# Kernel tuning notes

Measured on AMD Instinct MI355X. Metric: run time of the kernel, lower is better.

## Reference

```python
import jax, jax.numpy as jnp
import numpy as np

EPS = 1e-5
DOWNSAMPLE = 0.5


def setup_inputs() -> dict:
    key = jax.random.key(0)
    k1, k2, k3 = jax.random.split(key, 3)
    B, C, H, W = 32, 256, 128, 128
    x = jax.random.normal(k1, (B, C, H, W), dtype=jnp.float32)
    # 1x1 conv: weight [3, C], bias [3]
    conv_w = jax.random.normal(k2, (3, C), dtype=jnp.float32) / np.sqrt(C).astype(np.float32)
    conv_b = jax.random.normal(k3, (3,), dtype=jnp.float32) * 0.01
    return {"x": x, "conv_w": conv_w, "conv_b": conv_b}


def reference(x, conv_w, conv_b):
    B, C, H, W = x.shape
    dh = int(round(H * DOWNSAMPLE))
    dw = int(round(W * DOWNSAMPLE))

    # 1x1 conv producing 3 channels: 2 offset + 1 attention logit
    oa = jnp.einsum('bchw,oc->bohw', x, conv_w) + conv_b[None, :, None, None]
    offset = oa[:, :2]                      # [B,2,H,W]
    attention = jnp.exp(oa[:, 2:3])         # [B,1,H,W]

    # normalized destination coordinates = base grid + offset, clamped
    gy = jnp.broadcast_to((jnp.arange(H, dtype=x.dtype) / H)[:, None], (H, W))
    gx = jnp.broadcast_to((jnp.arange(W, dtype=x.dtype) / W)[None, :], (H, W))
    base = jnp.stack([gy, gx])              # [2,H,W]
    dest = jnp.clip(base[None] + offset, 0.0, 1.0 - EPS)
    dy = jnp.floor(dest[:, 0] * dh)
    dx = jnp.floor(dest[:, 1] * dw)
    cell = (dy * dw + dx).astype(jnp.int32)  # [B,H,W] spatial cell index

    # full flat destination index over (batch, channel, cell)
    b_off = jnp.arange(B, dtype=jnp.int32)[:, None, None, None] * (C * dh * dw)
    c_off = jnp.arange(C, dtype=jnp.int32)[None, :, None, None] * (dh * dw)
    destination = cell[:, None] + b_off + c_off  # [B,C,H,W]

    # scatter-add attention-weighted features
    xw = (x * attention).reshape(-1)
    feat = jax.ops.segment_sum(xw, destination.reshape(-1), num_segments=B * C * dh * dw)

    # scatter-add attention per (batch, cell) for normalization
    a_idx = cell + jnp.arange(B, dtype=jnp.int32)[:, None, None] * (dh * dw)
    att_sum = jax.ops.segment_sum(attention.reshape(-1), a_idx.reshape(-1), num_segments=B * dh * dw) + EPS

    out = feat.reshape(B, C, dh, dw) / att_sum.reshape(B, 1, dh, dw)
    return (out, offset, destination)
```

## Files before the change

kernel.cpp:

```cpp
#include <hip/hip_runtime.h>
#include <math.h>

#define NB 32
#define NC 256
#define NH 128
#define NW 128
#define NDH 64
#define NDW 64
#define NHW (NH * NW)
#define NCELLS (NDH * NDW)
#define OUT0_N (NB * NC * NCELLS)
#define OUT1_BASE OUT0_N
#define OUT1_N (NB * 2 * NHW)
#define OUT2_BASE (OUT1_BASE + OUT1_N)

#define EPSF 1e-5f

typedef unsigned short u16;
typedef unsigned int   u32;

#define WS_CELLS   ((size_t)0)
#define WS_ATTS    (WS_CELLS + (size_t)NB*NHW*2)
#define WS_ECOMB   (WS_ATTS + (size_t)NB*NHW*4)
#define WS_ASUM    (WS_ECOMB + (size_t)NB*NHW*4)

__global__ __launch_bounds__(256) void k_conv(
    const float* __restrict__ x, const float* __restrict__ cw,
    const float* __restrict__ cb, float* __restrict__ out,
    u16* __restrict__ cells, float* __restrict__ atts)
{
    __shared__ float cwS[3][NC];
    __shared__ float red[256][13];
    __shared__ int   cellv[64];

    const int t    = threadIdx.x;
    const int blk  = blockIdx.x;
    const int b    = blk >> 8;
    const int tile = blk & 255;
    const int h    = tile >> 1;
    const int w0   = (tile & 1) << 6;
    const int pixbase = h * NW + w0;

    cwS[0][t] = cw[t];
    cwS[1][t] = cw[NC + t];
    cwS[2][t] = cw[2 * NC + t];
    __syncthreads();

    const int ct = t >> 4;
    const int pg = (t & 15) << 2;
    const float* xb = x + (size_t)b * NC * NHW + pixbase + pg;

    float p00 = 0, p01 = 0, p02 = 0;
    float p10 = 0, p11 = 0, p12 = 0;
    float p20 = 0, p21 = 0, p22 = 0;
    float p30 = 0, p31 = 0, p32 = 0;

    #pragma unroll
    for (int i = 0; i < 16; ++i) {
        const int c = (i << 4) + ct;
        const float4 xv = *reinterpret_cast<const float4*>(xb + (size_t)c * NHW);
        const float wc0 = cwS[0][c], wc1 = cwS[1][c], wc2 = cwS[2][c];
        p00 += xv.x * wc0; p01 += xv.x * wc1; p02 += xv.x * wc2;
        p10 += xv.y * wc0; p11 += xv.y * wc1; p12 += xv.y * wc2;
        p20 += xv.z * wc0; p21 += xv.z * wc1; p22 += xv.z * wc2;
        p30 += xv.w * wc0; p31 += xv.w * wc1; p32 += xv.w * wc2;
    }

    red[t][0]  = p00; red[t][1]  = p01; red[t][2]  = p02;
    red[t][3]  = p10; red[t][4]  = p11; red[t][5]  = p12;
    red[t][6]  = p20; red[t][7]  = p21; red[t][8]  = p22;
    red[t][9]  = p30; red[t][10] = p31; red[t][11] = p32;
    __syncthreads();

    if (t < 64) {
        const int px   = t;
        const int row0 = px >> 2;
        const int col  = (px & 3) * 3;
        float s0 = 0, s1 = 0, s2 = 0;
        #pragma unroll
        for (int j = 0; j < 16; ++j) {
            const int r = row0 + (j << 4);
            s0 += red[r][col];
            s1 += red[r][col + 1];
            s2 += red[r][col + 2];
        }
        const float off0 = s0 + cb[0];
        const float off1 = s1 + cb[1];
        const float att  = expf(s2 + cb[2]);

        const float gy = (float)h * (1.0f / NH);
        const float gx = (float)(w0 + px) * (1.0f / NW);
        const float dyf = fminf(fmaxf(gy + off0, 0.0f), 0.99999f);
        const float dxf = fminf(fmaxf(gx + off1, 0.0f), 0.99999f);
        const int dy = (int)floorf(dyf * (float)NDH);
        const int dx = (int)floorf(dxf * (float)NDW);
        const int cell = dy * NDW + dx;

        cellv[px] = cell;
        cells[b * NHW + pixbase + px] = (u16)cell;
        atts [b * NHW + pixbase + px] = att;

        const int o1 = OUT1_BASE + b * 2 * NHW + pixbase + px;
        out[o1]       = off0;
        out[o1 + NHW] = off1;
    }
    __syncthreads();

    const int  c0 = cellv[pg], c1 = cellv[pg + 1], c2 = cellv[pg + 2], c3 = cellv[pg + 3];
    float* __restrict__ dst = out + OUT2_BASE;
    #pragma unroll
    for (int i = 0; i < 16; ++i) {
        const int c = (i << 4) + ct;
        const int basec = (b * NC + c) * NCELLS;
        float4 dv;
        dv.x = (float)(basec + c0);
        dv.y = (float)(basec + c1);
        dv.z = (float)(basec + c2);
        dv.w = (float)(basec + c3);
        *reinterpret_cast<float4*>(dst + (size_t)(b * NC + c) * NHW + pixbase + pg) = dv;
    }
}

__global__ __launch_bounds__(1024) void k_sort(
    const u16* __restrict__ cells, const float* __restrict__ atts,
    u32* __restrict__ ecomb, float* __restrict__ asum)
{
    __shared__ u32   hist[NCELLS];
    __shared__ float as_[NCELLS];
    __shared__ u32   ts[1024];

    const int t = threadIdx.x;
    const int b = blockIdx.x;
    const u16*   cb_ = cells + b * NHW;
    const float* ab_ = atts + b * NHW;

    #pragma unroll
    for (int j = 0; j < 4; ++j) { hist[t + 1024 * j] = 0u; as_[t + 1024 * j] = 0.f; }
    __syncthreads();

    #pragma unroll
    for (int j = 0; j < 16; ++j) {
        const int p  = t + 1024 * j;
        const int cl = cb_[p];
        atomicAdd(&hist[cl], 1u);
        atomicAdd(&as_[cl], ab_[p]);
    }
    __syncthreads();

    const u32 h0 = hist[4 * t], h1 = hist[4 * t + 1], h2 = hist[4 * t + 2], h3 = hist[4 * t + 3];
    const u32 T  = h0 + h1 + h2 + h3;
    ts[t] = T;
    __syncthreads();
    for (int off = 1; off < 1024; off <<= 1) {
        const u32 v = (t >= off) ? ts[t - off] : 0u;
        __syncthreads();
        ts[t] += v;
        __syncthreads();
    }
    const u32 base = ts[t] - T;
    hist[4 * t]     = base;
    hist[4 * t + 1] = base + h0;
    hist[4 * t + 2] = base + h0 + h1;
    hist[4 * t + 3] = base + h0 + h1 + h2;

    #pragma unroll
    for (int j = 0; j < 4; ++j)
        asum[b * NCELLS + t + 1024 * j] = as_[t + 1024 * j];
    __syncthreads();

    #pragma unroll
    for (int j = 0; j < 16; ++j) {
        const int p  = t + 1024 * j;
        const int cl = cb_[p];
        const u32 pos = atomicAdd(&hist[cl], 1u);
        ecomb[b * NHW + pos] = ((u32)cl << 16) | (u32)p;
    }
}

__global__ __launch_bounds__(256) void k_gather(
    const float* __restrict__ x, const float* __restrict__ atts,
    const u32* __restrict__ ecomb, const float* __restrict__ asum,
    float* __restrict__ out)
{
    __shared__ float xpl[NHW];
    __shared__ float acc[NCELLS];

    const int t   = threadIdx.x;
    const int blk = blockIdx.x;
    const int b   = blk >> 8;
    const int c   = blk & 255;

    const float4* xp4  = reinterpret_cast<const float4*>(x + (size_t)(b * NC + c) * NHW);
    const float4* at4  = reinterpret_cast<const float4*>(atts + b * NHW);
    float4*       xpl4 = reinterpret_cast<float4*>(xpl);
    float4*       acc4 = reinterpret_cast<float4*>(acc);

    #pragma unroll
    for (int k = 0; k < 16; ++k) {
        float4 xv = xp4[t + 256 * k];
        const float4 av = at4[t + 256 * k];
        xv.x *= av.x; xv.y *= av.y; xv.z *= av.z; xv.w *= av.w;
        xpl4[t + 256 * k] = xv;
    }
    const float4 z4 = make_float4(0.f, 0.f, 0.f, 0.f);
    #pragma unroll
    for (int k = 0; k < 4; ++k) acc4[t + 256 * k] = z4;
    __syncthreads();

    const u32* el = ecomb + b * NHW + t * 64;
    float s   = 0.f;
    int   cur = (int)(el[0] >> 16);

    #define ACCUM(E, V)                                            \
        {                                                          \
            const int cl_ = (int)((E) >> 16);                      \
            if (cl_ != cur) { atomicAdd(&acc[cur], s); s = 0.f; cur = cl_; } \
            s += (V);                                              \
        }

    for (int ch = 0; ch < 8; ++ch) {
        const uint4 e0 = *reinterpret_cast<const uint4*>(el + ch * 8);
        const uint4 e1 = *reinterpret_cast<const uint4*>(el + ch * 8 + 4);
        const float v0 = xpl[e0.x & 0xFFFFu];
        const float v1 = xpl[e0.y & 0xFFFFu];
        const float v2 = xpl[e0.z & 0xFFFFu];
        const float v3 = xpl[e0.w & 0xFFFFu];
        const float v4 = xpl[e1.x & 0xFFFFu];
        const float v5 = xpl[e1.y & 0xFFFFu];
        const float v6 = xpl[e1.z & 0xFFFFu];
        const float v7 = xpl[e1.w & 0xFFFFu];
        ACCUM(e0.x, v0); ACCUM(e0.y, v1); ACCUM(e0.z, v2); ACCUM(e0.w, v3);
        ACCUM(e1.x, v4); ACCUM(e1.y, v5); ACCUM(e1.z, v6); ACCUM(e1.w, v7);
    }
    atomicAdd(&acc[cur], s);
    #undef ACCUM
    __syncthreads();

    const float4* as4 = reinterpret_cast<const float4*>(asum + b * NCELLS);
    float4* ob4 = reinterpret_cast<float4*>(out + (size_t)(b * NC + c) * NCELLS);
    #pragma unroll
    for (int k = 0; k < 4; ++k) {
        float4 a = acc4[t + 256 * k];
        const float4 sv = as4[t + 256 * k];
        a.x /= (sv.x + EPSF);
        a.y /= (sv.y + EPSF);
        a.z /= (sv.z + EPSF);
        a.w /= (sv.w + EPSF);
        ob4[t + 256 * k] = a;
    }
}

extern "C" void kernel_launch(void* const* d_in, const int* in_sizes, int n_in,
                              void* d_out, int out_size, void* d_ws, size_t ws_size,
                              hipStream_t stream)
{
    (void)in_sizes; (void)n_in; (void)out_size; (void)ws_size;
    const float* x  = (const float*)d_in[0];
    const float* cw = (const float*)d_in[1];
    const float* cb = (const float*)d_in[2];
    float* out = (float*)d_out;
    char*  ws  = (char*)d_ws;

    u16*   cells = (u16*)  (ws + WS_CELLS);
    float* atts  = (float*)(ws + WS_ATTS);
    u32*   ecomb = (u32*)  (ws + WS_ECOMB);
    float* asum  = (float*)(ws + WS_ASUM);

    k_conv  <<<dim3(NB * 256), dim3(256),  0, stream>>>(x, cw, cb, out, cells, atts);
    k_sort  <<<dim3(NB),       dim3(1024), 0, stream>>>(cells, atts, ecomb, asum);
    k_gather<<<dim3(NB * NC),  dim3(256),  0, stream>>>(x, atts, ecomb, asum, out);
}
```

Before: 463.7 us.

## Stage x directly to LDS asynchronously and fold attention into sorted entries

The gather kernel now copies the x plane into LDS with global_load_lds instead of loading, multiplying by attention and storing through registers. The attention weight is packed next to each sorted entry (8-byte entries), so the multiply happens at gather time. The sort kernel precomputes the reciprocal of the attention sum, so the final normalisation is a multiply instead of a divide. Each thread also runs four independent accumulation streams for more ILP, at the cost of doubling entry-list bandwidth and adding more LDS atomics at stream boundaries.

```diff
diff --git a/kernel.cpp b/kernel.cpp
--- a/kernel.cpp
+++ b/kernel.cpp
@@ -21,8 +21,15 @@
 
 #define WS_CELLS   ((size_t)0)
 #define WS_ATTS    (WS_CELLS + (size_t)NB*NHW*2)
-#define WS_ECOMB   (WS_ATTS + (size_t)NB*NHW*4)
-#define WS_ASUM    (WS_ECOMB + (size_t)NB*NHW*4)
+#define WS_ENTS    (WS_ATTS + (size_t)NB*NHW*4)
+#define WS_IASUM   (WS_ENTS + (size_t)NB*NHW*8)
+
+__device__ __forceinline__ void async_stage16(const float* g, float* l) {
+    __builtin_amdgcn_global_load_lds(
+        (const __attribute__((address_space(1))) unsigned int*)g,
+        (__attribute__((address_space(3))) unsigned int*)l,
+        16, 0, 0);
+}
 
 __global__ __launch_bounds__(256) void k_conv(
     const float* __restrict__ x, const float* __restrict__ cw,
@@ -123,7 +130,7 @@
 
 __global__ __launch_bounds__(1024) void k_sort(
     const u16* __restrict__ cells, const float* __restrict__ atts,
-    u32* __restrict__ ecomb, float* __restrict__ asum)
+    uint2* __restrict__ ents, float* __restrict__ iasum)
 {
     __shared__ u32   hist[NCELLS];
     __shared__ float as_[NCELLS];
@@ -164,8 +171,10 @@
     hist[4 * t + 3] = base + h0 + h1 + h2;
 
     #pragma unroll
-    for (int j = 0; j < 4; ++j)
-        asum[b * NCELLS + t + 1024 * j] = as_[t + 1024 * j];
+    for (int j = 0; j < 4; ++j) {
+        const int i = t + 1024 * j;
+        iasum[b * NCELLS + i] = 1.0f / (as_[i] + EPSF);
+    }
     __syncthreads();
 
     #pragma unroll
@@ -173,79 +182,83 @@
         const int p  = t + 1024 * j;
         const int cl = cb_[p];
         const u32 pos = atomicAdd(&hist[cl], 1u);
-        ecomb[b * NHW + pos] = ((u32)cl << 16) | (u32)p;
-    }
-}
-
-__global__ __launch_bounds__(256) void k_gather(
-    const float* __restrict__ x, const float* __restrict__ atts,
-    const u32* __restrict__ ecomb, const float* __restrict__ asum,
-    float* __restrict__ out)
+        ents[b * NHW + pos] = make_uint2(((u32)cl << 16) | (u32)p,
+                                         __float_as_uint(ab_[p]));
+    }
+}
+
+#define ENT(EX, EY, CUR, S)                                                   \
+    {                                                                         \
+        const int   cl_ = (int)((EX) >> 16);                                  \
+        const float v_  = xpl[(EX) & 0xFFFFu] * __uint_as_float(EY);          \
+        if (cl_ != (CUR)) { atomicAdd(&acc[(CUR)], (S)); (S) = 0.f; (CUR) = cl_; } \
+        (S) += v_;                                                            \
+    }
+
+__global__ __launch_bounds__(256) void k_gd(
+    const float* __restrict__ x, const uint2* __restrict__ ents,
+    const float* __restrict__ iasum, float* __restrict__ out)
 {
     __shared__ float xpl[NHW];
     __shared__ float acc[NCELLS];
 
-    const int t   = threadIdx.x;
-    const int blk = blockIdx.x;
-    const int b   = blk >> 8;
-    const int c   = blk & 255;
-
-    const float4* xp4  = reinterpret_cast<const float4*>(x + (size_t)(b * NC + c) * NHW);
-    const float4* at4  = reinterpret_cast<const float4*>(atts + b * NHW);
-    float4*       xpl4 = reinterpret_cast<float4*>(xpl);
-    float4*       acc4 = reinterpret_cast<float4*>(acc);
-
+    const int t    = threadIdx.x;
+    const int blk  = blockIdx.x;
+    const int b    = blk >> 8;
+    const int c    = blk & 255;
+    const int wave = t >> 6;
+    const int lane = t & 63;
+
+    const float* xp = x + (size_t)(b * NC + c) * NHW;
     #pragma unroll
     for (int k = 0; k < 16; ++k) {
-        float4 xv = xp4[t + 256 * k];
-        const float4 av = at4[t + 256 * k];
-        xv.x *= av.x; xv.y *= av.y; xv.z *= av.z; xv.w *= av.w;
-        xpl4[t + 256 * k] = xv;
-    }
+        const int vec = (k * 4 + wave) * 64 + lane;
+        async_stage16(xp + vec * 4, &xpl[vec * 4]);
+    }
+
+    float4* acc4 = reinterpret_cast<float4*>(acc);
     const float4 z4 = make_float4(0.f, 0.f, 0.f, 0.f);
     #pragma unroll
     for (int k = 0; k < 4; ++k) acc4[t + 256 * k] = z4;
-    __syncthreads();
-
-    const u32* el = ecomb + b * NHW + t * 64;
-    float s   = 0.f;
-    int   cur = (int)(el[0] >> 16);
-
-    #define ACCUM(E, V)                                            \
-        {                                                          \
-            const int cl_ = (int)((E) >> 16);                      \
-            if (cl_ != cur) { atomicAdd(&acc[cur], s); s = 0.f; cur = cl_; } \
-            s += (V);                                              \
+
+    __syncthreads();
+
+    {
+        const uint2* el = ents + b * NHW + t * 64;
+        float s0 = 0.f, s1 = 0.f, s2 = 0.f, s3 = 0.f;
+        int   c0 = (int)(el[0].x  >> 16);
+        int   c1 = (int)(el[16].x >> 16);
+        int   c2 = (int)(el[32].x >> 16);
+        int   c3 = (int)(el[48].x >> 16);
+
+        #pragma unroll
+        for (int i = 0; i < 8; ++i) {
+            const uint4 q0 = *reinterpret_cast<const uint4*>(el + 0  + i * 2);
+            const uint4 q1 = *reinterpret_cast<const uint4*>(el + 16 + i * 2);
+            const uint4 q2 = *reinterpret_cast<const uint4*>(el + 32 + i * 2);
+            const uint4 q3 = *reinterpret_cast<const uint4*>(el + 48 + i * 2);
+            ENT(q0.x, q0.y, c0, s0); ENT(q0.z, q0.w, c0, s0);
+            ENT(q1.x, q1.y, c1, s1); ENT(q1.z, q1.w, c1, s1);
+            ENT(q2.x, q2.y, c2, s2); ENT(q2.z, q2.w, c2, s2);
+            ENT(q3.x, q3.y, c3, s3); ENT(q3.z, q3.w, c3, s3);
         }
-
-    for (int ch = 0; ch < 8; ++ch) {
-        const uint4 e0 = *reinterpret_cast<const uint4*>(el + ch * 8);
-        const uint4 e1 = *reinterpret_cast<const uint4*>(el + ch * 8 + 4);
-        const float v0 = xpl[e0.x & 0xFFFFu];
-        const float v1 = xpl[e0.y & 0xFFFFu];
-        const float v2 = xpl[e0.z & 0xFFFFu];
-        const float v3 = xpl[e0.w & 0xFFFFu];
-        const float v4 = xpl[e1.x & 0xFFFFu];
-        const float v5 = xpl[e1.y & 0xFFFFu];
-        const float v6 = xpl[e1.z & 0xFFFFu];
-        const float v7 = xpl[e1.w & 0xFFFFu];
-        ACCUM(e0.x, v0); ACCUM(e0.y, v1); ACCUM(e0.z, v2); ACCUM(e0.w, v3);
-        ACCUM(e1.x, v4); ACCUM(e1.y, v5); ACCUM(e1.z, v6); ACCUM(e1.w, v7);
-    }
-    atomicAdd(&acc[cur], s);
-    #undef ACCUM
-    __syncthreads();
-
-    const float4* as4 = reinterpret_cast<const float4*>(asum + b * NCELLS);
+        atomicAdd(&acc[c0], s0);
+        atomicAdd(&acc[c1], s1);
+        atomicAdd(&acc[c2], s2);
+        atomicAdd(&acc[c3], s3);
+    }
+    __syncthreads();
+
+    const float4* ia4 = reinterpret_cast<const float4*>(iasum + b * NCELLS);
     float4* ob4 = reinterpret_cast<float4*>(out + (size_t)(b * NC + c) * NCELLS);
     #pragma unroll
     for (int k = 0; k < 4; ++k) {
         float4 a = acc4[t + 256 * k];
-        const float4 sv = as4[t + 256 * k];
-        a.x /= (sv.x + EPSF);
-        a.y /= (sv.y + EPSF);
-        a.z /= (sv.z + EPSF);
-        a.w /= (sv.w + EPSF);
+        const float4 sv = ia4[t + 256 * k];
+        a.x *= sv.x;
+        a.y *= sv.y;
+        a.z *= sv.z;
+        a.w *= sv.w;
         ob4[t + 256 * k] = a;
     }
 }
@@ -263,10 +276,10 @@
 
     u16*   cells = (u16*)  (ws + WS_CELLS);
     float* atts  = (float*)(ws + WS_ATTS);
-    u32*   ecomb = (u32*)  (ws + WS_ECOMB);
-    float* asum  = (float*)(ws + WS_ASUM);
-
-    k_conv  <<<dim3(NB * 256), dim3(256),  0, stream>>>(x, cw, cb, out, cells, atts);
-    k_sort  <<<dim3(NB),       dim3(1024), 0, stream>>>(cells, atts, ecomb, asum);
-    k_gather<<<dim3(NB * NC),  dim3(256),  0, stream>>>(x, atts, ecomb, asum, out);
-}
+    uint2* ents  = (uint2*)(ws + WS_ENTS);
+    float* iasum = (float*)(ws + WS_IASUM);
+
+    k_conv<<<dim3(NB * 256), dim3(256),  0, stream>>>(x, cw, cb, out, cells, atts);
+    k_sort<<<dim3(NB),       dim3(1024), 0, stream>>>(cells, atts, ents, iasum);
+    k_gd  <<<dim3(NB * NC),  dim3(256),  0, stream>>>(x, ents, iasum, out);
+}
```

New measurement: 585.8 us. +26.3%, slower.
